# Kernel optimization log

Measured on AMD Instinct MI355X. Metric: run time of the kernel, lower is better.

## Reference

```python
import jax, jax.numpy as jnp
import numpy as np

B, N, D = 8, 2048, 64          # batch, n_pts, latent_ndim
K, S = 8, 256                   # n_clusters, book_size
TEMP = 0.5
EPS = 1e-10


def _gumbel(key, shape):
    U = jax.random.uniform(key, shape, dtype=jnp.float32)
    return -jnp.log(-jnp.log(U + EPS) + EPS)


def setup_inputs() -> dict:
    key = jax.random.key(0)
    k1, k2, k3 = jax.random.split(key, 3)
    return {
        "ze": jax.random.normal(k1, (B, N, D), jnp.float32),
        "c_logits": jax.random.normal(k2, (B, K), jnp.float32),
        "books": jax.random.normal(k3, (K, S, D), jnp.float32),
        "log_param_q": jnp.float32(0.0),       # log(param_q_init=1.0)
        "log_param_q_cls": jnp.float32(0.0),
        "is_train": 1,
    }


def reference(ze, c_logits, books, log_param_q, log_param_q_cls, is_train):
    b, n_pts, d = ze.shape
    k, s, _ = books.shape
    precision_q = 0.5 / jnp.clip(1.0 + jnp.exp(log_param_q), 1e-10)

    # pairwise squared distances: (b, k, n_pts, book_size)
    dist = ((ze ** 2).sum(-1)[:, None, :, None]
            + (books ** 2).sum(-1)[None, :, None, :]
            - 2.0 * jnp.einsum("bnd,ksd->bkns", ze, books))
    logit_k = -dist * precision_q  # (b, k, n, s)

    if is_train:
        precision_q_cls = 0.5 / jnp.clip(1.0 + jnp.exp(log_param_q_cls), 1e-10)
        nkey = jax.random.key(42)
        g_cls = _gumbel(jax.random.fold_in(nkey, 0), (b, k))
        g_enc = _gumbel(jax.random.fold_in(nkey, 1), (b, k, n_pts, s))
        # gumbel-softmax over clusters
        c_prob = jax.nn.softmax((c_logits * precision_q_cls + g_cls) / TEMP, axis=-1)  # (b,k)
        # mixture of per-cluster logits
        logits = jnp.einsum("bkns,bk->bns", logit_k, c_prob)
        # gumbel-softmax relaxed codebook assignment per cluster
        enc = jax.nn.softmax((logit_k + g_enc) / TEMP, axis=-1)  # (b,k,n,s)
        zq = jnp.einsum("bkns,ksd,bk->bnd", enc, books, c_prob)
    else:
        idx = jnp.argmax(c_logits, axis=-1)                 # (b,)
        sel_books = books[idx]                              # (b,s,d)
        logits = jnp.take_along_axis(logit_k, idx[:, None, None, None], axis=1)[:, 0]  # (b,n,s)
        code = jnp.argmax(logits, axis=-1)                  # (b,n)
        zq = jnp.take_along_axis(sel_books, code[..., None], axis=1)  # hard lookup (b,n,d)

    prob = jax.nn.softmax(logits, axis=-1)
    log_prob = jax.nn.log_softmax(logits, axis=-1)
    return zq, precision_q, prob, log_prob
```

## Files before the change

### kernel.cpp

```cpp
#include <hip/hip_runtime.h>
#include <cstdint>
#include <cstddef>


#define B_ 8
#define N_ 2048
#define D_ 64
#define K_ 8
#define S_ 256
#define ROWS 16

#define ZQ_ELEMS   (B_ * N_ * D_)
#define PROB_ELEMS (B_ * N_ * S_)

typedef __attribute__((ext_vector_type(8))) short short8;
typedef __attribute__((ext_vector_type(4))) float f32x4;

struct U2 { unsigned a, b; };

__host__ __device__ constexpr U2 tf2x32(unsigned k0, unsigned k1, unsigned x0, unsigned x1) {
  unsigned ks2 = k0 ^ k1 ^ 0x1BD11BDAu;
#define TFR(r) x0 += x1; x1 = (x1 << (r)) | (x1 >> (32 - (r))); x1 ^= x0;
  x0 += k0; x1 += k1;
  TFR(13) TFR(15) TFR(26) TFR(6)
  x0 += k1;  x1 += ks2 + 1u;
  TFR(17) TFR(29) TFR(16) TFR(24)
  x0 += ks2; x1 += k0 + 2u;
  TFR(13) TFR(15) TFR(26) TFR(6)
  x0 += k0;  x1 += k1 + 3u;
  TFR(17) TFR(29) TFR(16) TFR(24)
  x0 += k1;  x1 += ks2 + 4u;
  TFR(13) TFR(15) TFR(26) TFR(6)
  x0 += ks2; x1 += k0 + 5u;
#undef TFR
  return U2{x0, x1};
}

constexpr U2 KCLS = tf2x32(0u, 42u, 0u, 0u);
constexpr U2 KENC = tf2x32(0u, 42u, 0u, 1u);

__device__ __forceinline__ unsigned tf_bits(unsigned k0, unsigned k1, unsigned i) {
  unsigned ks2 = k0 ^ k1 ^ 0x1BD11BDAu;
  unsigned x0 = 0u, x1 = i;
#define TFRD(r) x0 += x1; x1 = __builtin_rotateleft32(x1, r); x1 ^= x0;
  x0 += k0; x1 += k1;
  TFRD(13) TFRD(15) TFRD(26) TFRD(6)
  x0 += k1;  x1 += ks2 + 1u;
  TFRD(17) TFRD(29) TFRD(16) TFRD(24)
  x0 += ks2; x1 += k0 + 2u;
  TFRD(13) TFRD(15) TFRD(26) TFRD(6)
  x0 += k0;  x1 += k1 + 3u;
  TFRD(17) TFRD(29) TFRD(16) TFRD(24)
  x0 += k1;  x1 += ks2 + 4u;
  TFRD(13) TFRD(15) TFRD(26) TFRD(6)
  x0 += ks2; x1 += k0 + 5u;
#undef TFRD
  return x0 ^ x1;
}

__device__ __forceinline__ float bits_to_u01(unsigned bits) {
  return __uint_as_float((bits >> 9) | 0x3f800000u) - 1.0f;
}

__device__ __forceinline__ unsigned short f2bf(float f) {
  unsigned u = __float_as_uint(f);
  unsigned r = (u + 0x7FFFu + ((u >> 16) & 1u)) >> 16;
  return (unsigned short)r;
}
__device__ __forceinline__ float bf2f(unsigned short h) {
  return __uint_as_float(((unsigned)h) << 16);
}

__global__ void k_prep(const float* __restrict__ books,
                       const float* __restrict__ c_logits,
                       const float* __restrict__ lpq,
                       const float* __restrict__ lpq_cls,
                       float* __restrict__ pq_out,
                       float* __restrict__ cprob_ws,
                       float* __restrict__ b2_ws,
                       ushort* __restrict__ bkhi, ushort* __restrict__ bklo,
                       ushort* __restrict__ bkT) {
  __shared__ ushort lds_t[64][68];
  __shared__ float g[64];
  const int tid = threadIdx.x;

  if (blockIdx.x < 32) {
    const int kk = blockIdx.x >> 2;
    const int st0 = (blockIdx.x & 3) * 64;
    const int sl = tid >> 2, dq = tid & 3;
    const float* src = books + ((size_t)(kk * 256 + st0 + sl)) * D_ + dq * 16;
    float f[16];
    #pragma unroll
    for (int j = 0; j < 4; ++j) {
      float4 v = *(const float4*)(src + j * 4);
      f[j*4+0] = v.x; f[j*4+1] = v.y; f[j*4+2] = v.z; f[j*4+3] = v.w;
    }
    float q = 0.0f;
    #pragma unroll
    for (int i = 0; i < 16; ++i) q = fmaf(f[i], f[i], q);
    q += __shfl_xor(q, 1); q += __shfl_xor(q, 2);
    if (dq == 0) b2_ws[kk * 256 + st0 + sl] = q;

    ushort hi[16], lo[16];
    #pragma unroll
    for (int i = 0; i < 16; ++i) {
      hi[i] = f2bf(f[i]);
      lo[i] = f2bf(f[i] - bf2f(hi[i]));
    }
    const size_t obase = ((size_t)(kk * 256 + st0 + sl)) * D_ + dq * 16;
    #pragma unroll
    for (int j = 0; j < 4; ++j) {
      ushort4 h4, l4;
      h4.x = hi[j*4+0]; h4.y = hi[j*4+1]; h4.z = hi[j*4+2]; h4.w = hi[j*4+3];
      l4.x = lo[j*4+0]; l4.y = lo[j*4+1]; l4.z = lo[j*4+2]; l4.w = lo[j*4+3];
      *(ushort4*)(bkhi + obase + j * 4) = h4;
      *(ushort4*)(bklo + obase + j * 4) = l4;
      *(ushort4*)&lds_t[sl][dq * 16 + j * 4] = h4;
    }
    __syncthreads();
    const int dl = tid >> 2, s4 = tid & 3;
    ushort* dst = bkT + ((size_t)(kk * 64 + dl)) * S_ + st0 + s4 * 16;
    #pragma unroll
    for (int j = 0; j < 4; ++j) {
      ushort4 o;
      o.x = lds_t[s4*16 + j*4 + 0][dl];
      o.y = lds_t[s4*16 + j*4 + 1][dl];
      o.z = lds_t[s4*16 + j*4 + 2][dl];
      o.w = lds_t[s4*16 + j*4 + 3][dl];
      *(ushort4*)(dst + j * 4) = o;
    }
  } else {
    if (tid == 0) pq_out[0] = 0.5f / fmaxf(1.0f + expf(lpq[0]), 1e-10f);
    const float pq_cls = 0.5f / fmaxf(1.0f + expf(lpq_cls[0]), 1e-10f);
    if (tid < 64) {
      unsigned bits = tf_bits(KCLS.a, KCLS.b, (unsigned)tid);
      float u = bits_to_u01(bits);
      g[tid] = -logf(-logf(u + 1e-10f) + 1e-10f);
    }
    __syncthreads();
    if (tid < 64) {
      float v = (c_logits[tid] * pq_cls + g[tid]) * 2.0f;
      float M = v;
      #pragma unroll
      for (int m = 1; m < 8; m <<= 1) M = fmaxf(M, __shfl_xor(M, m, 8));
      float e = expf(v - M);
      float Z = e;
      #pragma unroll
      for (int m = 1; m < 8; m <<= 1) Z += __shfl_xor(Z, m, 8);
      cprob_ws[tid] = e / Z;
    }
  }
}

__global__ __launch_bounds__(512, 8) void k_main(
    const float* __restrict__ ze,
    const ushort* __restrict__ bkhi, const ushort* __restrict__ bklo,
    const ushort* __restrict__ bkT,
    const float* __restrict__ lpq, const float* __restrict__ cprob_ws,
    const float* __restrict__ b2_ws,
    float* __restrict__ zq_out, float* __restrict__ prob_out,
    float* __restrict__ logp_out) {

  __shared__ __align__(16) ushort zeh_s[ROWS][72];
  __shared__ __align__(16) ushort zel_s[ROWS][72];
  __shared__ __align__(16) ushort enc_s[ROWS][264];
  __shared__ __align__(16) float b2_s[K_ * S_];
  __shared__ __align__(16) float red_s[ROWS][8];
  __shared__ __align__(16) float m_s[ROWS][8];
  __shared__ __align__(16) float z_s[ROWS][8];
  __shared__ __align__(16) float zq_red[ROWS][68];
  __shared__ float q2_s[ROWS];
  __shared__ float cp_s[8];

  const int tid = threadIdx.x;
  const int b   = blockIdx.y;
  const int n0  = blockIdx.x * ROWS;
  const int w   = tid >> 6;
  const int l   = tid & 63;
  const int llo = l & 15;
  const int lhi = l >> 4;
  const int s0  = w * 32;
  const int d0  = (w >> 1) * 16;
  const int sh  = w & 1;

  const float pq = 0.5f / fmaxf(1.0f + expf(lpq[0]), 1e-10f);

  if (tid < 256) {
    const int row = tid >> 4, d4 = (tid & 15) * 4;
    float4 v = *(const float4*)(ze + ((size_t)(b * N_ + n0 + row)) * D_ + d4);
    float q = v.x * v.x + v.y * v.y + v.z * v.z + v.w * v.w;
    q += __shfl_xor(q, 1); q += __shfl_xor(q, 2);
    q += __shfl_xor(q, 4); q += __shfl_xor(q, 8);
    if ((tid & 15) == 0) q2_s[row] = q;
    float f[4] = {v.x, v.y, v.z, v.w};
    ushort4 hh, ll4;
    ushort* hp = (ushort*)&hh; ushort* lp = (ushort*)&ll4;
    #pragma unroll
    for (int i = 0; i < 4; ++i) {
      unsigned short hb = f2bf(f[i]);
      hp[i] = hb;
      lp[i] = f2bf(f[i] - bf2f(hb));
    }
    *(ushort4*)&zeh_s[row][d4] = hh;
    *(ushort4*)&zel_s[row][d4] = ll4;
  }
  {
    float4 bv = *(const float4*)(b2_ws + tid * 4);
    *(float4*)&b2_s[tid * 4] = bv;
  }
  if (tid < 8) cp_s[tid] = cprob_ws[b * 8 + tid];
  __syncthreads();

  const short8 ah0 = *(const short8*)&zeh_s[llo][lhi * 8];
  const short8 ah1 = *(const short8*)&zeh_s[llo][32 + lhi * 8];
  const short8 al0 = *(const short8*)&zel_s[llo][lhi * 8];
  const short8 al1 = *(const short8*)&zel_s[llo][32 + lhi * 8];

  float lacc[2][4];
  #pragma unroll
  for (int nt = 0; nt < 2; ++nt)
    #pragma unroll
    for (int r = 0; r < 4; ++r) lacc[nt][r] = 0.0f;
  f32x4 zqacc = {0.f, 0.f, 0.f, 0.f};

  for (int cb = 0; cb < K_; ++cb) {
    const ushort* bp = bkhi + cb * (S_ * D_) + (size_t)(s0 + llo) * D_ + lhi * 8;
    const ushort* bq = bklo + cb * (S_ * D_) + (size_t)(s0 + llo) * D_ + lhi * 8;

    f32x4 acc[2];
    acc[0] = (f32x4){0.f, 0.f, 0.f, 0.f};
    acc[1] = (f32x4){0.f, 0.f, 0.f, 0.f};
    #pragma unroll
    for (int nt = 0; nt < 2; ++nt) {
      const ushort* p = bp + nt * (16 * D_);
      const ushort* q = bq + nt * (16 * D_);
      short8 b0 = *(const short8*)p;
      short8 b1 = *(const short8*)(p + 32);
      short8 c0 = *(const short8*)q;
      short8 c1 = *(const short8*)(q + 32);
      acc[nt] = __builtin_amdgcn_mfma_f32_16x16x32_bf16(ah0, b0, acc[nt], 0, 0, 0);
      acc[nt] = __builtin_amdgcn_mfma_f32_16x16x32_bf16(ah1, b1, acc[nt], 0, 0, 0);
      acc[nt] = __builtin_amdgcn_mfma_f32_16x16x32_bf16(al0, b0, acc[nt], 0, 0, 0);
      acc[nt] = __builtin_amdgcn_mfma_f32_16x16x32_bf16(al1, b1, acc[nt], 0, 0, 0);
      acc[nt] = __builtin_amdgcn_mfma_f32_16x16x32_bf16(ah0, c0, acc[nt], 0, 0, 0);
      acc[nt] = __builtin_amdgcn_mfma_f32_16x16x32_bf16(ah1, c1, acc[nt], 0, 0, 0);
    }

    const float cpk = cp_s[cb];
    float b2v[2];
    b2v[0] = b2_s[cb * 256 + s0 + llo];
    b2v[1] = b2_s[cb * 256 + s0 + 16 + llo];
    float ev[4][2];
    #pragma unroll
    for (int r = 0; r < 4; ++r) {
      const int rowg = lhi * 4 + r;
      const float q2 = q2_s[rowg];
      const unsigned ib =
          (((unsigned)(b * 8 + cb)) << 19) | (((unsigned)(n0 + rowg)) << 8);
      float Zp = 0.0f;
      #pragma unroll
      for (int nt = 0; nt < 2; ++nt) {
        float dist = q2 + b2v[nt] - 2.0f * acc[nt][r];
        float lk = -pq * dist;
        lacc[nt][r] = fmaf(cpk, lk, lacc[nt][r]);
        unsigned bits = tf_bits(KENC.a, KENC.b, ib | (unsigned)(s0 + nt * 16 + llo));
        float u = bits_to_u01(bits);
        float wv = 0.0f - __logf(u + 1e-10f);
        float t = wv + 1e-10f;
        float ex = __expf(fmaf(2.0f, lk, 40.0f));
        float e = __fdividef(ex, t * t);
        ev[r][nt] = e;
        Zp += e;
      }
      Zp += __shfl_xor(Zp, 1); Zp += __shfl_xor(Zp, 2);
      Zp += __shfl_xor(Zp, 4); Zp += __shfl_xor(Zp, 8);
      if (llo == 0) red_s[rowg][w] = Zp;
    }
    __syncthreads();

    #pragma unroll
    for (int r = 0; r < 4; ++r) {
      const int rowg = lhi * 4 + r;
      const float4 z0 = *(const float4*)&red_s[rowg][0];
      const float4 z1 = *(const float4*)&red_s[rowg][4];
      float Z = ((z0.x + z0.y) + (z0.z + z0.w)) + ((z1.x + z1.y) + (z1.z + z1.w));
      const float sc = __fdividef(cpk, Z);
      enc_s[rowg][s0 + llo]      = f2bf(ev[r][0] * sc);
      enc_s[rowg][s0 + 16 + llo] = f2bf(ev[r][1] * sc);
    }
    __syncthreads();

    {
      const ushort* bt = bkT + (size_t)cb * (D_ * S_) +
                         (size_t)(d0 + llo) * S_ + sh * 128 + lhi * 8;
      #pragma unroll
      for (int sc4 = 0; sc4 < 4; ++sc4) {
        short8 af = *(const short8*)&enc_s[llo][sh * 128 + sc4 * 32 + lhi * 8];
        short8 bf = *(const short8*)(bt + sc4 * 32);
        zqacc = __builtin_amdgcn_mfma_f32_16x16x32_bf16(af, bf, zqacc, 0, 0, 0);
      }
    }
    __syncthreads();
  }

  #pragma unroll
  for (int r = 0; r < 4; ++r) {
    const int rowg = lhi * 4 + r;
    if (sh == 0) zq_red[rowg][d0 + llo] = zqacc[r];
    float Mp = fmaxf(lacc[0][r], lacc[1][r]);
    Mp = fmaxf(Mp, __shfl_xor(Mp, 1)); Mp = fmaxf(Mp, __shfl_xor(Mp, 2));
    Mp = fmaxf(Mp, __shfl_xor(Mp, 4)); Mp = fmaxf(Mp, __shfl_xor(Mp, 8));
    if (llo == 0) m_s[rowg][w] = Mp;
  }
  __syncthreads();
  float Mfull[4];
  #pragma unroll
  for (int r = 0; r < 4; ++r) {
    const int rowg = lhi * 4 + r;
    const float4 m0 = *(const float4*)&m_s[rowg][0];
    const float4 m1 = *(const float4*)&m_s[rowg][4];
    const float M = fmaxf(fmaxf(fmaxf(m0.x, m0.y), fmaxf(m0.z, m0.w)),
                          fmaxf(fmaxf(m1.x, m1.y), fmaxf(m1.z, m1.w)));
    Mfull[r] = M;
    float Zp = __expf(lacc[0][r] - M) + __expf(lacc[1][r] - M);
    Zp += __shfl_xor(Zp, 1); Zp += __shfl_xor(Zp, 2);
    Zp += __shfl_xor(Zp, 4); Zp += __shfl_xor(Zp, 8);
    if (llo == 0) z_s[rowg][w] = Zp;
    if (sh == 1) {
      float vzq = zq_red[rowg][d0 + llo] + zqacc[r];
      zq_out[((size_t)(b * N_ + n0 + rowg)) * D_ + d0 + llo] = vzq;
    }
  }
  __syncthreads();
  #pragma unroll
  for (int r = 0; r < 4; ++r) {
    const int rowg = lhi * 4 + r;
    const float M = Mfull[r];
    const float4 z0 = *(const float4*)&z_s[rowg][0];
    const float4 z1 = *(const float4*)&z_s[rowg][4];
    float Z = ((z0.x + z0.y) + (z0.z + z0.w)) + ((z1.x + z1.y) + (z1.z + z1.w));
    const float inv = __fdividef(1.0f, Z);
    const float lZ = __logf(Z);
    const size_t base = ((size_t)(b * N_ + n0 + rowg)) * S_ + s0 + llo;
    #pragma unroll
    for (int nt = 0; nt < 2; ++nt) {
      const float lmm = lacc[nt][r] - M;
      prob_out[base + nt * 16] = __expf(lmm) * inv;
      logp_out[base + nt * 16] = lmm - lZ;
    }
  }
}

extern "C" void kernel_launch(void* const* d_in, const int* in_sizes, int n_in,
                              void* d_out, int out_size, void* d_ws, size_t ws_size,
                              hipStream_t stream) {
  const float* ze    = (const float*)d_in[0];
  const float* clog  = (const float*)d_in[1];
  const float* books = (const float*)d_in[2];
  const float* lpq   = (const float*)d_in[3];
  const float* lpqc  = (const float*)d_in[4];

  float* out      = (float*)d_out;
  float* zq_out   = out;
  float* pq_out   = out + ZQ_ELEMS;
  float* prob_out = out + ZQ_ELEMS + 1;
  float* logp_out = out + ZQ_ELEMS + 1 + PROB_ELEMS;

  float* wsf    = (float*)d_ws;
  float* cprob  = wsf;
  float* b2     = wsf + 64;
  ushort* bkhi  = (ushort*)(wsf + 2112);
  ushort* bklo  = bkhi + (K_ * S_ * D_);
  ushort* bkT   = bklo + (K_ * S_ * D_);

  hipLaunchKernelGGL(k_prep, dim3(33), dim3(256), 0, stream,
                     books, clog, lpq, lpqc, pq_out, cprob, b2, bkhi, bklo, bkT);
  hipLaunchKernelGGL(k_main, dim3(128, 8), dim3(512), 0, stream,
                     ze, bkhi, bklo, bkT, lpq, cprob, b2, zq_out, prob_out, logp_out);
}
```

Before: 240.2 us.

## Double rows per block, defer softmax normalization past zq MFMA, use nontemporal IO

```diff
diff --git a/kernel.cpp b/kernel.cpp
--- a/kernel.cpp
+++ b/kernel.cpp
@@ -8,7 +8,7 @@
 #define D_ 64
 #define K_ 8
 #define S_ 256
-#define ROWS 16
+#define ROWS 32
 
 #define ZQ_ELEMS   (B_ * N_ * D_)
 #define PROB_ELEMS (B_ * N_ * S_)
@@ -152,7 +152,7 @@
   }
 }
 
-__global__ __launch_bounds__(512, 8) void k_main(
+__global__ __launch_bounds__(1024, 8) void k_main(
     const float* __restrict__ ze,
     const ushort* __restrict__ bkhi, const ushort* __restrict__ bklo,
     const ushort* __restrict__ bkT,
@@ -179,20 +179,23 @@
   const int l   = tid & 63;
   const int llo = l & 15;
   const int lhi = l >> 4;
-  const int s0  = w * 32;
-  const int d0  = (w >> 1) * 16;
-  const int sh  = w & 1;
+  const int h   = w & 1;
+  const int j   = w >> 1;
+  const int s0  = j * 32;
+  const int d0  = (j >> 1) * 16;
+  const int sh  = j & 1;
 
   const float pq = 0.5f / fmaxf(1.0f + expf(lpq[0]), 1e-10f);
 
-  if (tid < 256) {
+  if (tid < 512) {
     const int row = tid >> 4, d4 = (tid & 15) * 4;
-    float4 v = *(const float4*)(ze + ((size_t)(b * N_ + n0 + row)) * D_ + d4);
-    float q = v.x * v.x + v.y * v.y + v.z * v.z + v.w * v.w;
+    f32x4 vv = __builtin_nontemporal_load(
+        (const f32x4*)(ze + ((size_t)(b * N_ + n0 + row)) * D_ + d4));
+    float q = vv[0] * vv[0] + vv[1] * vv[1] + vv[2] * vv[2] + vv[3] * vv[3];
     q += __shfl_xor(q, 1); q += __shfl_xor(q, 2);
     q += __shfl_xor(q, 4); q += __shfl_xor(q, 8);
     if ((tid & 15) == 0) q2_s[row] = q;
-    float f[4] = {v.x, v.y, v.z, v.w};
+    float f[4] = {vv[0], vv[1], vv[2], vv[3]};
     ushort4 hh, ll4;
     ushort* hp = (ushort*)&hh; ushort* lp = (ushort*)&ll4;
     #pragma unroll
@@ -203,18 +206,18 @@
     }
     *(ushort4*)&zeh_s[row][d4] = hh;
     *(ushort4*)&zel_s[row][d4] = ll4;
-  }
-  {
-    float4 bv = *(const float4*)(b2_ws + tid * 4);
-    *(float4*)&b2_s[tid * 4] = bv;
+  } else {
+    const int idx = tid - 512;
+    float4 bv = *(const float4*)(b2_ws + idx * 4);
+    *(float4*)&b2_s[idx * 4] = bv;
   }
   if (tid < 8) cp_s[tid] = cprob_ws[b * 8 + tid];
   __syncthreads();
 
-  const short8 ah0 = *(const short8*)&zeh_s[llo][lhi * 8];
-  const short8 ah1 = *(const short8*)&zeh_s[llo][32 + lhi * 8];
-  const short8 al0 = *(const short8*)&zel_s[llo][lhi * 8];
-  const short8 al1 = *(const short8*)&zel_s[llo][32 + lhi * 8];
+  const short8 ah0 = *(const short8*)&zeh_s[h * 16 + llo][lhi * 8];
+  const short8 ah1 = *(const short8*)&zeh_s[h * 16 + llo][32 + lhi * 8];
+  const short8 al0 = *(const short8*)&zel_s[h * 16 + llo][lhi * 8];
+  const short8 al1 = *(const short8*)&zel_s[h * 16 + llo][32 + lhi * 8];
 
   float lacc[2][4];
   #pragma unroll
@@ -250,14 +253,13 @@
     float b2v[2];
     b2v[0] = b2_s[cb * 256 + s0 + llo];
     b2v[1] = b2_s[cb * 256 + s0 + 16 + llo];
-    float ev[4][2];
     #pragma unroll
     for (int r = 0; r < 4; ++r) {
-      const int rowg = lhi * 4 + r;
+      const int rowg = h * 16 + lhi * 4 + r;
       const float q2 = q2_s[rowg];
       const unsigned ib =
           (((unsigned)(b * 8 + cb)) << 19) | (((unsigned)(n0 + rowg)) << 8);
-      float Zp = 0.0f;
+      float e[2];
       #pragma unroll
       for (int nt = 0; nt < 2; ++nt) {
         float dist = q2 + b2v[nt] - 2.0f * acc[nt][r];
@@ -268,36 +270,34 @@
         float wv = 0.0f - __logf(u + 1e-10f);
         float t = wv + 1e-10f;
         float ex = __expf(fmaf(2.0f, lk, 40.0f));
-        float e = __fdividef(ex, t * t);
-        ev[r][nt] = e;
-        Zp += e;
+        e[nt] = __fdividef(ex, t * t);
       }
+      float Zp = e[0] + e[1];
       Zp += __shfl_xor(Zp, 1); Zp += __shfl_xor(Zp, 2);
       Zp += __shfl_xor(Zp, 4); Zp += __shfl_xor(Zp, 8);
-      if (llo == 0) red_s[rowg][w] = Zp;
-    }
-    __syncthreads();
-
-    #pragma unroll
-    for (int r = 0; r < 4; ++r) {
-      const int rowg = lhi * 4 + r;
-      const float4 z0 = *(const float4*)&red_s[rowg][0];
-      const float4 z1 = *(const float4*)&red_s[rowg][4];
-      float Z = ((z0.x + z0.y) + (z0.z + z0.w)) + ((z1.x + z1.y) + (z1.z + z1.w));
-      const float sc = __fdividef(cpk, Z);
-      enc_s[rowg][s0 + llo]      = f2bf(ev[r][0] * sc);
-      enc_s[rowg][s0 + 16 + llo] = f2bf(ev[r][1] * sc);
+      if (llo == 0) red_s[rowg][j] = Zp;
+      enc_s[rowg][s0 + llo]      = f2bf(e[0]);
+      enc_s[rowg][s0 + 16 + llo] = f2bf(e[1]);
     }
     __syncthreads();
 
     {
       const ushort* bt = bkT + (size_t)cb * (D_ * S_) +
                          (size_t)(d0 + llo) * S_ + sh * 128 + lhi * 8;
+      f32x4 zqp = {0.f, 0.f, 0.f, 0.f};
       #pragma unroll
       for (int sc4 = 0; sc4 < 4; ++sc4) {
-        short8 af = *(const short8*)&enc_s[llo][sh * 128 + sc4 * 32 + lhi * 8];
+        short8 af = *(const short8*)&enc_s[h * 16 + llo][sh * 128 + sc4 * 32 + lhi * 8];
         short8 bf = *(const short8*)(bt + sc4 * 32);
-        zqacc = __builtin_amdgcn_mfma_f32_16x16x32_bf16(af, bf, zqacc, 0, 0, 0);
+        zqp = __builtin_amdgcn_mfma_f32_16x16x32_bf16(af, bf, zqp, 0, 0, 0);
+      }
+      #pragma unroll
+      for (int r = 0; r < 4; ++r) {
+        const int rowg = h * 16 + lhi * 4 + r;
+        const float4 z0 = *(const float4*)&red_s[rowg][0];
+        const float4 z1 = *(const float4*)&red_s[rowg][4];
+        float Z = ((z0.x + z0.y) + (z0.z + z0.w)) + ((z1.x + z1.y) + (z1.z + z1.w));
+        zqacc[r] = fmaf(__fdividef(cpk, Z), zqp[r], zqacc[r]);
       }
     }
     __syncthreads();
@@ -305,18 +305,19 @@
 
   #pragma unroll
   for (int r = 0; r < 4; ++r) {
-    const int rowg = lhi * 4 + r;
+    const int rowg = h * 16 + lhi * 4 + r;
     if (sh == 0) zq_red[rowg][d0 + llo] = zqacc[r];
     float Mp = fmaxf(lacc[0][r], lacc[1][r]);
     Mp = fmaxf(Mp, __shfl_xor(Mp, 1)); Mp = fmaxf(Mp, __shfl_xor(Mp, 2));
     Mp = fmaxf(Mp, __shfl_xor(Mp, 4)); Mp = fmaxf(Mp, __shfl_xor(Mp, 8));
-    if (llo == 0) m_s[rowg][w] = Mp;
+    if (llo == 0) m_s[rowg][j] = Mp;
   }
   __syncthreads();
+
   float Mfull[4];
   #pragma unroll
   for (int r = 0; r < 4; ++r) {
-    const int rowg = lhi * 4 + r;
+    const int rowg = h * 16 + lhi * 4 + r;
     const float4 m0 = *(const float4*)&m_s[rowg][0];
     const float4 m1 = *(const float4*)&m_s[rowg][4];
     const float M = fmaxf(fmaxf(fmaxf(m0.x, m0.y), fmaxf(m0.z, m0.w)),
@@ -325,16 +326,18 @@
     float Zp = __expf(lacc[0][r] - M) + __expf(lacc[1][r] - M);
     Zp += __shfl_xor(Zp, 1); Zp += __shfl_xor(Zp, 2);
     Zp += __shfl_xor(Zp, 4); Zp += __shfl_xor(Zp, 8);
-    if (llo == 0) z_s[rowg][w] = Zp;
+    if (llo == 0) z_s[rowg][j] = Zp;
     if (sh == 1) {
       float vzq = zq_red[rowg][d0 + llo] + zqacc[r];
-      zq_out[((size_t)(b * N_ + n0 + rowg)) * D_ + d0 + llo] = vzq;
+      __builtin_nontemporal_store(
+          vzq, zq_out + ((size_t)(b * N_ + n0 + rowg)) * D_ + d0 + llo);
     }
   }
   __syncthreads();
+
   #pragma unroll
   for (int r = 0; r < 4; ++r) {
-    const int rowg = lhi * 4 + r;
+    const int rowg = h * 16 + lhi * 4 + r;
     const float M = Mfull[r];
     const float4 z0 = *(const float4*)&z_s[rowg][0];
     const float4 z1 = *(const float4*)&z_s[rowg][4];
@@ -345,8 +348,8 @@
     #pragma unroll
     for (int nt = 0; nt < 2; ++nt) {
       const float lmm = lacc[nt][r] - M;
-      prob_out[base + nt * 16] = __expf(lmm) * inv;
-      logp_out[base + nt * 16] = lmm - lZ;
+      __builtin_nontemporal_store(__expf(lmm) * inv, prob_out + base + nt * 16);
+      __builtin_nontemporal_store(lmm - lZ, logp_out + base + nt * 16);
     }
   }
 }
@@ -375,6 +378,6 @@
 
   hipLaunchKernelGGL(k_prep, dim3(33), dim3(256), 0, stream,
                      books, clog, lpq, lpqc, pq_out, cprob, b2, bkhi, bklo, bkT);
-  hipLaunchKernelGGL(k_main, dim3(128, 8), dim3(512), 0, stream,
+  hipLaunchKernelGGL(k_main, dim3(64, 8), dim3(1024), 0, stream,
                      ze, bkhi, bklo, bkT, lpq, cprob, b2, zq_out, prob_out, logp_out);
 }
```

Measured after the change: 255.8 us. +6.5%, slower.
